# Kernel optimization log

Hardware: AMD Instinct MI355X
Metric: run time of the kernel (lower is better)

Reference implementation:

```python
import jax, jax.numpy as jnp
import numpy as np

IN_SIZE = 128
OUT_SIZE = 128
NEG_SLOPE = 0.01  # flax.nnx.leaky_relu default


def setup_inputs() -> dict:
    key = jax.random.key(0)
    x = jax.random.normal(key, (8, IN_SIZE, IN_SIZE, 128), dtype=jnp.float32)
    return {"x": x}


def reference(x) -> jnp.ndarray:
    b, _, _, c = x.shape
    x = jax.image.resize(x, (b, 2 * IN_SIZE, 2 * IN_SIZE, c), method='bicubic', antialias=True)
    # filtered nonlinearity
    x = jax.nn.leaky_relu(x, negative_slope=NEG_SLOPE)
    # bicubic antialiased downsample back to out_size
    x = jax.image.resize(x, (b, OUT_SIZE, OUT_SIZE, c), method='bicubic', antialias=True)
    return x
```

## Files before the change

### kernel.cpp

```cpp
#include <hip/hip_runtime.h>

typedef float f2 __attribute__((ext_vector_type(2)));
typedef float f4 __attribute__((ext_vector_type(4)));

#define IN_H 128
#define IN_W 128
#define NCH  128
#define UPN  256

constexpr int SEG  = 8;
constexpr int COLS = 32;
constexpr int CH   = 32;
constexpr int IRW  = 14;
constexpr int ICW  = 38;
constexpr int NT4  = IRW * ICW * CH / 4;

__device__ __forceinline__ float cubic_k(float x) {
  float r = 0.f;
  if (x < 1.f)      r = (1.5f * x - 2.5f) * x * x + 1.f;
  else if (x < 2.f) r = ((-0.5f * x + 2.5f) * x - 4.f) * x + 2.f;
  return r;
}

#define GLDS(g, l)                                                         \
  __builtin_amdgcn_global_load_lds(                                        \
      (const __attribute__((address_space(1))) void*)(g),                  \
      (__attribute__((address_space(3))) void*)(l), 16, 0, 0)

__global__ __launch_bounds__(256, 2)
void actfilter_kernel(const float* __restrict__ x, float* __restrict__ out) {
  __shared__ __align__(16) float xin[IRW][ICW][CH];
  __shared__ __align__(16) float upw[UPN][4];
  __shared__ __align__(16) float dww[IN_H][8];

  const int tid = threadIdx.x;

  int bid  = blockIdx.x;
  int work = ((bid & 7) << 8) | (bid >> 3);
  const int b   = work >> 8;
  const int rs  = (work >> 4) & 15;
  const int cs  = (work >> 2) & 3;
  const int chs = work & 3;
  const int i0  = rs * SEG;
  const int jc0 = cs * COLS;
  const int c0  = chs * CH;
  const int mlo = i0 - 3;
  const int mhi = i0 + 10;

  const float* xbase = x   + (size_t)b * IN_H * IN_W * NCH;
  float*       obase = out + (size_t)b * IN_H * IN_W * NCH;

  {
    char* lbase = (char*)&xin[0][0][0] + ((tid >> 6) << 10);
#pragma unroll
    for (int pass = 0; pass < 17; ++pass) {
      int t = tid + pass * 256;
      if (t < NT4) {
        int row   = t / 304;
        int rem   = t - row * 304;
        int col   = rem >> 3;
        int piece = rem & 7;
        int gr = min(max(mlo + row, 0), IN_H - 1);
        int gc = min(max(jc0 - 3 + col, 0), IN_W - 1);
        const float* gp = xbase + ((size_t)gr * IN_W + gc) * NCH + c0 + piece * 4;
        GLDS(gp, lbase + pass * 4096);
      }
    }
  }

  {
    int o = tid;
    int k = o >> 1;
    int base = (o & 1) ? (k - 1) : (k - 2);
    float s = 0.5f * o - 0.25f;
    float w[4]; float sum = 0.f;
#pragma unroll
    for (int t = 0; t < 4; ++t) {
      int tap = base + t;
      float wt = (tap >= 0 && tap < IN_H) ? cubic_k(fabsf(s - (float)tap)) : 0.f;
      w[t] = wt; sum += wt;
    }
    float inv = 1.f / sum;
#pragma unroll
    for (int t = 0; t < 4; ++t) upw[o][t] = w[t] * inv;
  }
  if (tid < IN_H) {
    int j = tid;
    float s = 2.f * j + 0.5f;
    float w[8]; float sum = 0.f;
#pragma unroll
    for (int t = 0; t < 8; ++t) {
      int tap = 2 * j - 3 + t;
      float wt = (tap >= 0 && tap < UPN) ? cubic_k(0.5f * fabsf(s - (float)tap)) : 0.f;
      w[t] = wt; sum += wt;
    }
    float inv = 1.f / sum;
#pragma unroll
    for (int t = 0; t < 8; ++t) dww[j][t] = w[t] * inv;
  }

  __syncthreads();

  const int cp = tid >> 4;
  const int e  = tid & 15;
  const int j0 = jc0 + 2 * cp;

  f4 wvv[10];
#pragma unroll
  for (int c = 0; c < 10; ++c) {
    int cu = min(max(2 * j0 - 3 + c, 0), UPN - 1);
    wvv[c] = *(const f4*)&upw[cu][0];
  }
  float dw0[8], dw1[8];
  {
    f4 a = *(const f4*)&dww[j0][0],     bq = *(const f4*)&dww[j0][4];
    f4 c2 = *(const f4*)&dww[j0 + 1][0], d = *(const f4*)&dww[j0 + 1][4];
#pragma unroll
    for (int t = 0; t < 4; ++t) {
      dw0[t] = a[t]; dw0[t + 4] = bq[t];
      dw1[t] = c2[t]; dw1[t + 4] = d[t];
    }
  }

  const int r_lo = max(2 * i0 - 3, 0);
  const int r_hi = min(2 * i0 + 2 * SEG + 2, UPN - 1);

  f2 tw[4][10];
  f2 accA[4], accB[4];
#pragma unroll
  for (int s2 = 0; s2 < 4; ++s2) {
    accA[s2] = (f2){0.f, 0.f};
    accB[s2] = (f2){0.f, 0.f};
  }

#define DO_R(RV, S0, S1, S2, S3)                                             \
  do {                                                                       \
    int r = (RV);                                                            \
    if (r >= r_lo && r <= r_hi) {                                            \
      f4 wh = *(const f4*)&upw[r][0];                                        \
      f2 z0 = (f2){0.f, 0.f}, z1 = (f2){0.f, 0.f};                           \
      _Pragma("unroll")                                                      \
      for (int c = 0; c < 10; ++c) {                                         \
        f2 hu = wh.x * tw[S0][c] + wh.y * tw[S1][c]                          \
              + wh.z * tw[S2][c] + wh.w * tw[S3][c];                         \
        f2 lv;                                                               \
        lv.x = fmaxf(hu.x, 0.01f * hu.x);                                    \
        lv.y = fmaxf(hu.y, 0.01f * hu.y);                                    \
        if (c < 8)  z0 += dw0[c] * lv;                                       \
        if (c >= 2) z1 += dw1[c - 2] * lv;                                   \
      }                                                                      \
      int ilo = max(i0, (r - 3) >> 1);                                       \
      int ihi = min(i0 + SEG - 1, (r + 3) >> 1);                             \
      _Pragma("unroll")                                                      \
      for (int s = 0; s < 4; ++s) {                                          \
        int i = ilo + ((s - ilo) & 3);                                       \
        if (i <= ihi) {                                                      \
          float w = dww[i][r - 2 * i + 3];                                   \
          accA[s] += w * z0;                                                 \
          accB[s] += w * z1;                                                 \
          bool done = (r == 2 * i + 4) ||                                    \
                      (r == UPN - 1 && 2 * i + 4 > UPN - 1);                 \
          if (done) {                                                        \
            float* dst = obase + ((size_t)i * IN_W + j0) * NCH + c0 + 2 * e; \
            *(f2*)dst         = accA[s];                                     \
            *(f2*)(dst + NCH) = accB[s];                                     \
            accA[s] = (f2){0.f, 0.f};                                        \
            accB[s] = (f2){0.f, 0.f};                                        \
          }                                                                  \
        }                                                                    \
      }                                                                      \
    }                                                                        \
  } while (0)

#define STEP(PH)                                                             \
  do {                                                                       \
    int m = mlo + mb + (PH);                                                 \
    if (m <= mhi) {                                                          \
      int ml = m - mlo;                                                      \
      f2 raw[8];                                                             \
      _Pragma("unroll")                                                      \
      for (int k = 0; k < 8; ++k)                                            \
        raw[k] = *(const f2*)&xin[ml][2 * cp + k][2 * e];                    \
      _Pragma("unroll")                                                      \
      for (int c = 0; c < 10; ++c) {                                         \
        tw[(PH) & 3][c] = wvv[c].x * raw[(c >> 1) + 0]                       \
                        + wvv[c].y * raw[(c >> 1) + 1]                       \
                        + wvv[c].z * raw[(c >> 1) + 2]                       \
                        + wvv[c].w * raw[(c >> 1) + 3];                      \
      }                                                                      \
      DO_R(2 * m - 3, ((PH) + 1) & 3, ((PH) + 2) & 3, ((PH) + 3) & 3, (PH) & 3); \
      DO_R(2 * m - 2, ((PH) + 1) & 3, ((PH) + 2) & 3, ((PH) + 3) & 3, (PH) & 3); \
    }                                                                        \
  } while (0)

  for (int mb = 0; mb < 16; mb += 4) {
    STEP(0);
    STEP(1);
    STEP(2);
    STEP(3);
  }

#undef STEP
#undef DO_R
}

extern "C" void kernel_launch(void* const* d_in, const int* in_sizes, int n_in,
                              void* d_out, int out_size, void* d_ws, size_t ws_size,
                              hipStream_t stream) {
  const float* x = (const float*)d_in[0];
  float* out = (float*)d_out;
  actfilter_kernel<<<dim3(2048), dim3(256), 0, stream>>>(x, out);
}
```

Before: 75.61 us.

## Compute upsample and activation stages in packed fp16 with fp16 LDS tile

Converts the input tile to fp16 when staging it into shared memory (padded channel stride), and runs the horizontal/vertical upsample, leaky ReLU and horizontal downsample in packed half2 arithmetic, with fp32 accumulation only for the final vertical pass. The direct global-to-LDS loads are replaced by register-staged loads interleaved with weight setup, and launch bounds go up to three blocks per SM. This is meant to halve LDS footprint and ALU work through packed math, at the cost of fp16 rounding error in the intermediate values, which may exceed tolerance.

```diff
diff --git a/kernel.cpp b/kernel.cpp
--- a/kernel.cpp
+++ b/kernel.cpp
@@ -2,6 +2,7 @@
 
 typedef float f2 __attribute__((ext_vector_type(2)));
 typedef float f4 __attribute__((ext_vector_type(4)));
+typedef _Float16 h2 __attribute__((ext_vector_type(2)));
 
 #define IN_H 128
 #define IN_W 128
@@ -11,9 +12,11 @@
 constexpr int SEG  = 8;
 constexpr int COLS = 32;
 constexpr int CH   = 32;
+constexpr int CHP  = 40;
 constexpr int IRW  = 14;
 constexpr int ICW  = 38;
 constexpr int NT4  = IRW * ICW * CH / 4;
+constexpr int TPR  = ICW * CH / 4;
 
 __device__ __forceinline__ float cubic_k(float x) {
   float r = 0.f;
@@ -22,14 +25,18 @@
   return r;
 }
 
-#define GLDS(g, l)                                                         \
-  __builtin_amdgcn_global_load_lds(                                        \
-      (const __attribute__((address_space(1))) void*)(g),                  \
-      (__attribute__((address_space(3))) void*)(l), 16, 0, 0)
-
-__global__ __launch_bounds__(256, 2)
+__device__ __forceinline__ h2 splat_h(float w) {
+  h2 r; r.x = (_Float16)w; r.y = (_Float16)w; return r;
+}
+
+__device__ __forceinline__ h2 pkrtz(float a, float b) {
+  auto t = __builtin_amdgcn_cvt_pkrtz(a, b);
+  return __builtin_bit_cast(h2, t);
+}
+
+__global__ __launch_bounds__(256, 3)
 void actfilter_kernel(const float* __restrict__ x, float* __restrict__ out) {
-  __shared__ __align__(16) float xin[IRW][ICW][CH];
+  __shared__ __align__(16) _Float16 xin[IRW][ICW][CHP];
   __shared__ __align__(16) float upw[UPN][4];
   __shared__ __align__(16) float dww[IN_H][8];
 
@@ -50,23 +57,48 @@
   const float* xbase = x   + (size_t)b * IN_H * IN_W * NCH;
   float*       obase = out + (size_t)b * IN_H * IN_W * NCH;
 
-  {
-    char* lbase = (char*)&xin[0][0][0] + ((tid >> 6) << 10);
-#pragma unroll
-    for (int pass = 0; pass < 17; ++pass) {
-      int t = tid + pass * 256;
-      if (t < NT4) {
-        int row   = t / 304;
-        int rem   = t - row * 304;
-        int col   = rem >> 3;
-        int piece = rem & 7;
-        int gr = min(max(mlo + row, 0), IN_H - 1);
-        int gc = min(max(jc0 - 3 + col, 0), IN_W - 1);
-        const float* gp = xbase + ((size_t)gr * IN_W + gc) * NCH + c0 + piece * 4;
-        GLDS(gp, lbase + pass * 4096);
+  auto ldb = [&](int bb, f4* v) {
+#pragma unroll
+    for (int k = 0; k < 6; ++k) {
+      int idx = bb * 6 + k;
+      if (idx < 17) {
+        int t = tid + idx * 256;
+        if (t < NT4) {
+          int row   = t / TPR;
+          int rem   = t - row * TPR;
+          int col   = rem >> 3;
+          int piece = rem & 7;
+          int gr = min(max(mlo + row, 0), IN_H - 1);
+          int gc = min(max(jc0 - 3 + col, 0), IN_W - 1);
+          v[k] = *(const f4*)(xbase + ((size_t)gr * IN_W + gc) * NCH
+                              + c0 + piece * 4);
+        }
       }
     }
-  }
+  };
+  auto stb = [&](int bb, const f4* v) {
+#pragma unroll
+    for (int k = 0; k < 6; ++k) {
+      int idx = bb * 6 + k;
+      if (idx < 17) {
+        int t = tid + idx * 256;
+        if (t < NT4) {
+          int row   = t / TPR;
+          int rem   = t - row * TPR;
+          int col   = rem >> 3;
+          int piece = rem & 7;
+          h2 lo = pkrtz(v[k].x, v[k].y);
+          h2 hi = pkrtz(v[k].z, v[k].w);
+          _Float16* lp = &xin[row][col][piece * 4];
+          *(h2*)lp       = lo;
+          *(h2*)(lp + 2) = hi;
+        }
+      }
+    }
+  };
+
+  f4 va[6], vb[6];
+  ldb(0, va);
 
   {
     int o = tid;
@@ -99,33 +131,39 @@
     for (int t = 0; t < 8; ++t) dww[j][t] = w[t] * inv;
   }
 
+  ldb(1, vb);
+  stb(0, va);
+  ldb(2, va);
+  stb(1, vb);
+  stb(2, va);
+
   __syncthreads();
 
   const int cp = tid >> 4;
   const int e  = tid & 15;
   const int j0 = jc0 + 2 * cp;
 
-  f4 wvv[10];
+  h2 wvv[10][4];
 #pragma unroll
   for (int c = 0; c < 10; ++c) {
     int cu = min(max(2 * j0 - 3 + c, 0), UPN - 1);
-    wvv[c] = *(const f4*)&upw[cu][0];
-  }
-  float dw0[8], dw1[8];
-  {
-    f4 a = *(const f4*)&dww[j0][0],     bq = *(const f4*)&dww[j0][4];
-    f4 c2 = *(const f4*)&dww[j0 + 1][0], d = *(const f4*)&dww[j0 + 1][4];
-#pragma unroll
-    for (int t = 0; t < 4; ++t) {
-      dw0[t] = a[t]; dw0[t + 4] = bq[t];
-      dw1[t] = c2[t]; dw1[t + 4] = d[t];
-    }
+#pragma unroll
+    for (int t = 0; t < 4; ++t) wvv[c][t] = splat_h(upw[cu][t]);
+  }
+  h2 dwA[8], dwB[8];
+#pragma unroll
+  for (int t = 0; t < 8; ++t) {
+    dwA[t] = splat_h(dww[j0][t]);
+    dwB[t] = splat_h(dww[j0 + 1][t]);
   }
 
   const int r_lo = max(2 * i0 - 3, 0);
   const int r_hi = min(2 * i0 + 2 * SEG + 2, UPN - 1);
 
-  f2 tw[4][10];
+  const h2 k01   = splat_h(0.01f);
+  const h2 hzero = splat_h(0.f);
+
+  h2 tw[4][10];
   f2 accA[4], accB[4];
 #pragma unroll
   for (int s2 = 0; s2 < 4; ++s2) {
@@ -137,18 +175,21 @@
   do {                                                                       \
     int r = (RV);                                                            \
     if (r >= r_lo && r <= r_hi) {                                            \
-      f4 wh = *(const f4*)&upw[r][0];                                        \
-      f2 z0 = (f2){0.f, 0.f}, z1 = (f2){0.f, 0.f};                           \
+      h2 wh0 = splat_h(upw[r][0]);                                           \
+      h2 wh1 = splat_h(upw[r][1]);                                           \
+      h2 wh2 = splat_h(upw[r][2]);                                           \
+      h2 wh3 = splat_h(upw[r][3]);                                           \
+      h2 z0 = hzero, z1 = hzero;                                             \
       _Pragma("unroll")                                                      \
       for (int c = 0; c < 10; ++c) {                                         \
-        f2 hu = wh.x * tw[S0][c] + wh.y * tw[S1][c]                          \
-              + wh.z * tw[S2][c] + wh.w * tw[S3][c];                         \
-        f2 lv;                                                               \
-        lv.x = fmaxf(hu.x, 0.01f * hu.x);                                    \
-        lv.y = fmaxf(hu.y, 0.01f * hu.y);                                    \
-        if (c < 8)  z0 += dw0[c] * lv;                                       \
-        if (c >= 2) z1 += dw1[c - 2] * lv;                                   \
+        h2 hu = wh0 * tw[S0][c] + wh1 * tw[S1][c]                            \
+              + wh2 * tw[S2][c] + wh3 * tw[S3][c];                           \
+        h2 lv = __builtin_elementwise_max(hu, hu * k01);                     \
+        if (c < 8)  z0 += dwA[c] * lv;                                       \
+        if (c >= 2) z1 += dwB[c - 2] * lv;                                   \
       }                                                                      \
+      f2 zf0 = (f2){(float)z0.x, (float)z0.y};                               \
+      f2 zf1 = (f2){(float)z1.x, (float)z1.y};                               \
       int ilo = max(i0, (r - 3) >> 1);                                       \
       int ihi = min(i0 + SEG - 1, (r + 3) >> 1);                             \
       _Pragma("unroll")                                                      \
@@ -156,8 +197,8 @@
         int i = ilo + ((s - ilo) & 3);                                       \
         if (i <= ihi) {                                                      \
           float w = dww[i][r - 2 * i + 3];                                   \
-          accA[s] += w * z0;                                                 \
-          accB[s] += w * z1;                                                 \
+          accA[s] += w * zf0;                                                \
+          accB[s] += w * zf1;                                                \
           bool done = (r == 2 * i + 4) ||                                    \
                       (r == UPN - 1 && 2 * i + 4 > UPN - 1);                 \
           if (done) {                                                        \
@@ -177,16 +218,16 @@
     int m = mlo + mb + (PH);                                                 \
     if (m <= mhi) {                                                          \
       int ml = m - mlo;                                                      \
-      f2 raw[8];                                                             \
+      h2 raw[8];                                                             \
       _Pragma("unroll")                                                      \
       for (int k = 0; k < 8; ++k)                                            \
-        raw[k] = *(const f2*)&xin[ml][2 * cp + k][2 * e];                    \
+        raw[k] = *(const h2*)&xin[ml][2 * cp + k][2 * e];                    \
       _Pragma("unroll")                                                      \
       for (int c = 0; c < 10; ++c) {                                         \
-        tw[(PH) & 3][c] = wvv[c].x * raw[(c >> 1) + 0]                       \
-                        + wvv[c].y * raw[(c >> 1) + 1]                       \
-                        + wvv[c].z * raw[(c >> 1) + 2]                       \
-                        + wvv[c].w * raw[(c >> 1) + 3];                      \
+        tw[(PH) & 3][c] = wvv[c][0] * raw[(c >> 1) + 0]                      \
+                        + wvv[c][1] * raw[(c >> 1) + 1]                      \
+                        + wvv[c][2] * raw[(c >> 1) + 2]                      \
+                        + wvv[c][3] * raw[(c >> 1) + 3];                     \
       }                                                                      \
       DO_R(2 * m - 3, ((PH) + 1) & 3, ((PH) + 2) & 3, ((PH) + 3) & 3, (PH) & 3); \
       DO_R(2 * m - 2, ((PH) + 1) & 3, ((PH) + 2) & 3, ((PH) + 3) & 3, (PH) & 3); \
```

Result: slower. 119.5 us (+58.1%).

## Compute upsample and nonlinearity in packed fp16 with constant interior weights

Applied to the files above, without the earlier changes.

Converts the horizontal and vertical upsample taps, the leaky-relu and the horizontal downsample partial sums to packed half-precision FMAs. Inputs are converted with round-toward-zero packing, and only the final vertical downsample accumulation stays in fp32. Interior vertical upsample weights are replaced with compile-time constants, so the per-row LDS weight load only happens at the image edges. The aim is to double ALU throughput on the dominant inner loops, at the cost of fp16 rounding error that may exceed tolerance.

```diff
diff --git a/kernel.cpp b/kernel.cpp
--- a/kernel.cpp
+++ b/kernel.cpp
@@ -2,6 +2,7 @@
 
 typedef float f2 __attribute__((ext_vector_type(2)));
 typedef float f4 __attribute__((ext_vector_type(4)));
+typedef _Float16 h2 __attribute__((ext_vector_type(2)));
 
 #define IN_H 128
 #define IN_W 128
@@ -21,6 +22,14 @@
   else if (x < 2.f) r = ((-0.5f * x + 2.5f) * x - 4.f) * x + 2.f;
   return r;
 }
+
+__device__ __forceinline__ h2 pkrtz(float a, float b) {
+  auto t = __builtin_amdgcn_cvt_pkrtz(a, b);
+  return __builtin_bit_cast(h2, t);
+}
+__device__ __forceinline__ h2 hsplat(float w) { return pkrtz(w, w); }
+
+#define HFMA(a, b, c) __builtin_elementwise_fma((a), (b), (c))
 
 #define GLDS(g, l)                                                         \
   __builtin_amdgcn_global_load_lds(                                        \
@@ -105,27 +114,33 @@
   const int e  = tid & 15;
   const int j0 = jc0 + 2 * cp;
 
-  f4 wvv[10];
+  h2 wvh[10][4];
 #pragma unroll
   for (int c = 0; c < 10; ++c) {
     int cu = min(max(2 * j0 - 3 + c, 0), UPN - 1);
-    wvv[c] = *(const f4*)&upw[cu][0];
-  }
-  float dw0[8], dw1[8];
+    f4 wf = *(const f4*)&upw[cu][0];
+    wvh[c][0] = hsplat(wf.x); wvh[c][1] = hsplat(wf.y);
+    wvh[c][2] = hsplat(wf.z); wvh[c][3] = hsplat(wf.w);
+  }
+  h2 dh0[8], dh1[8];
   {
     f4 a = *(const f4*)&dww[j0][0],     bq = *(const f4*)&dww[j0][4];
     f4 c2 = *(const f4*)&dww[j0 + 1][0], d = *(const f4*)&dww[j0 + 1][4];
 #pragma unroll
     for (int t = 0; t < 4; ++t) {
-      dw0[t] = a[t]; dw0[t + 4] = bq[t];
-      dw1[t] = c2[t]; dw1[t + 4] = d[t];
+      dh0[t] = hsplat(a[t]); dh0[t + 4] = hsplat(bq[t]);
+      dh1[t] = hsplat(c2[t]); dh1[t + 4] = hsplat(d[t]);
     }
   }
 
   const int r_lo = max(2 * i0 - 3, 0);
   const int r_hi = min(2 * i0 + 2 * SEG + 2, UPN - 1);
 
-  f2 tw[4][10];
+  const h2 whE0 = hsplat(-0.0234375f), whE1 = hsplat(0.2265625f),
+           whE2 = hsplat(0.8671875f),  whE3 = hsplat(-0.0703125f);
+  const h2 k01h = hsplat(0.01f);
+
+  h2 tw[4][10];
   f2 accA[4], accB[4];
 #pragma unroll
   for (int s2 = 0; s2 < 4; ++s2) {
@@ -133,22 +148,28 @@
     accB[s2] = (f2){0.f, 0.f};
   }
 
-#define DO_R(RV, S0, S1, S2, S3)                                             \
+#define DO_R(RV, W0, W1, W2, W3, S0, S1, S2, S3)                             \
   do {                                                                       \
     int r = (RV);                                                            \
     if (r >= r_lo && r <= r_hi) {                                            \
-      f4 wh = *(const f4*)&upw[r][0];                                        \
-      f2 z0 = (f2){0.f, 0.f}, z1 = (f2){0.f, 0.f};                           \
+      h2 w0 = (W0), w1 = (W1), w2 = (W2), w3 = (W3);                         \
+      if (r < 3 || r > 252) {                                                \
+        f4 wf = *(const f4*)&upw[r][0];                                      \
+        w0 = hsplat(wf.x); w1 = hsplat(wf.y);                                \
+        w2 = hsplat(wf.z); w3 = hsplat(wf.w);                                \
+      }                                                                      \
+      h2 z0 = hsplat(0.f), z1 = hsplat(0.f);                                 \
       _Pragma("unroll")                                                      \
       for (int c = 0; c < 10; ++c) {                                         \
-        f2 hu = wh.x * tw[S0][c] + wh.y * tw[S1][c]                          \
-              + wh.z * tw[S2][c] + wh.w * tw[S3][c];                         \
-        f2 lv;                                                               \
-        lv.x = fmaxf(hu.x, 0.01f * hu.x);                                    \
-        lv.y = fmaxf(hu.y, 0.01f * hu.y);                                    \
-        if (c < 8)  z0 += dw0[c] * lv;                                       \
-        if (c >= 2) z1 += dw1[c - 2] * lv;                                   \
-      }                                                                      \
+        h2 hu = HFMA(w0, tw[S0][c],                                          \
+                HFMA(w1, tw[S1][c],                                          \
+                HFMA(w2, tw[S2][c], w3 * tw[S3][c])));                       \
+        h2 lv = __builtin_elementwise_max(hu, hu * k01h);                    \
+        if (c < 8)  z0 = HFMA(dh0[c], lv, z0);                               \
+        if (c >= 2) z1 = HFMA(dh1[c - 2], lv, z1);                           \
+      }                                                                      \
+      f2 zf0; zf0.x = (float)z0.x; zf0.y = (float)z0.y;                      \
+      f2 zf1; zf1.x = (float)z1.x; zf1.y = (float)z1.y;                      \
       int ilo = max(i0, (r - 3) >> 1);                                       \
       int ihi = min(i0 + SEG - 1, (r + 3) >> 1);                             \
       _Pragma("unroll")                                                      \
@@ -156,8 +177,8 @@
         int i = ilo + ((s - ilo) & 3);                                       \
         if (i <= ihi) {                                                      \
           float w = dww[i][r - 2 * i + 3];                                   \
-          accA[s] += w * z0;                                                 \
-          accB[s] += w * z1;                                                 \
+          accA[s] += w * zf0;                                                \
+          accB[s] += w * zf1;                                                \
           bool done = (r == 2 * i + 4) ||                                    \
                       (r == UPN - 1 && 2 * i + 4 > UPN - 1);                 \
           if (done) {                                                        \
@@ -177,19 +198,23 @@
     int m = mlo + mb + (PH);                                                 \
     if (m <= mhi) {                                                          \
       int ml = m - mlo;                                                      \
-      f2 raw[8];                                                             \
-      _Pragma("unroll")                                                      \
-      for (int k = 0; k < 8; ++k)                                            \
-        raw[k] = *(const f2*)&xin[ml][2 * cp + k][2 * e];                    \
+      h2 raw[8];                                                             \
+      _Pragma("unroll")                                                      \
+      for (int k = 0; k < 8; ++k) {                                          \
+        f2 rv = *(const f2*)&xin[ml][2 * cp + k][2 * e];                     \
+        raw[k] = pkrtz(rv.x, rv.y);                                          \
+      }                                                                      \
       _Pragma("unroll")                                                      \
       for (int c = 0; c < 10; ++c) {                                         \
-        tw[(PH) & 3][c] = wvv[c].x * raw[(c >> 1) + 0]                       \
-                        + wvv[c].y * raw[(c >> 1) + 1]                       \
-                        + wvv[c].z * raw[(c >> 1) + 2]                       \
-                        + wvv[c].w * raw[(c >> 1) + 3];                      \
-      }                                                                      \
-      DO_R(2 * m - 3, ((PH) + 1) & 3, ((PH) + 2) & 3, ((PH) + 3) & 3, (PH) & 3); \
-      DO_R(2 * m - 2, ((PH) + 1) & 3, ((PH) + 2) & 3, ((PH) + 3) & 3, (PH) & 3); \
+        tw[(PH) & 3][c] = HFMA(wvh[c][0], raw[(c >> 1) + 0],                 \
+                          HFMA(wvh[c][1], raw[(c >> 1) + 1],                 \
+                          HFMA(wvh[c][2], raw[(c >> 1) + 2],                 \
+                               wvh[c][3] * raw[(c >> 1) + 3])));             \
+      }                                                                      \
+      DO_R(2 * m - 3, whE3, whE2, whE1, whE0,                                \
+           ((PH) + 1) & 3, ((PH) + 2) & 3, ((PH) + 3) & 3, (PH) & 3);        \
+      DO_R(2 * m - 2, whE0, whE1, whE2, whE3,                                \
+           ((PH) + 1) & 3, ((PH) + 2) & 3, ((PH) + 3) & 3, (PH) & 3);        \
     }                                                                        \
   } while (0)
 
```

New measurement: 89.95 us. 19.0% more time.
